# Optimization experiments

Hardware: AMD Instinct MI355X
Metric: run time of the kernel (lower is better)

The kernel has to match this reference:

```python
import jax, jax.numpy as jnp
import numpy as np

GROUPS = 32
EPS = 1e-6


def group_norm(x, gamma, beta):
    # x: [B,H,W,C], NHWC group norm with 32 groups (tfa.layers.GroupNormalization)
    B, H, W, C = x.shape
    g = x.reshape(B, H, W, GROUPS, C // GROUPS)
    mean = g.mean(axis=(1, 2, 4), keepdims=True)
    var = g.var(axis=(1, 2, 4), keepdims=True)
    g = (g - mean) * jax.lax.rsqrt(var + EPS)
    return g.reshape(B, H, W, C) * gamma + beta


def setup_inputs() -> dict:
    key = jax.random.key(0)
    ks = jax.random.split(key, 8)
    B, H, W, C = 8, 64, 64, 64
    s = 1.0 / np.sqrt(C)
    return {
        "x": jax.random.normal(ks[0], (B, H, W, C), jnp.float32),
        "gamma": jnp.ones((C,), jnp.float32),
        "beta": jnp.zeros((C,), jnp.float32),
        "Wq": jax.random.normal(ks[1], (C, C), jnp.float32) * s,
        "bq": jnp.zeros((C,), jnp.float32),
        "Wk": jax.random.normal(ks[2], (C, C), jnp.float32) * s,
        "bk": jnp.zeros((C,), jnp.float32),
        "Wv": jax.random.normal(ks[3], (C, C), jnp.float32) * s,
        "bv": jnp.zeros((C,), jnp.float32),
        "Wp": jax.random.normal(ks[4], (C, C), jnp.float32) * s,
        "bp": jnp.zeros((C,), jnp.float32),
    }


def reference(x, gamma, beta, Wq, bq, Wk, bk, Wv, bv, Wp, bp):
    B, H, W, C = x.shape
    h = group_norm(x, gamma, beta)
    q = h @ Wq + bq            # 1x1 conv (nin) projections, [B,H,W,C]
    k = h @ Wk + bk
    v = h @ Wv + bv
    scale = jnp.asarray(C, x.dtype) ** -0.5
    # full spatial self-attention over flattened HW grid
    w = jnp.einsum('bhwc,bHWc->bhwHW', q, k) * scale
    w = jax.nn.softmax(w.reshape(B, H, W, H * W), axis=-1).reshape(B, H, W, H, W)
    h = jnp.einsum('bhwHW,bHWc->bhwc', w, v)
    h = h @ Wp + bp
    return x + h
```

## Files before the change

### kernel.cpp

```cpp
#include <hip/hip_runtime.h>


typedef __bf16 bf16x8 __attribute__((ext_vector_type(8)));
typedef float f32x16 __attribute__((ext_vector_type(16)));
typedef unsigned u32x2 __attribute__((ext_vector_type(2)));

static __device__ __forceinline__ unsigned short f2b(float f) {
  union { __bf16 b; unsigned short u; } c; c.b = (__bf16)f; return c.u;
}
static __device__ __forceinline__ float b2f(unsigned short u) {
  union { float f; unsigned u; } c; c.u = ((unsigned)u) << 16; return c.f;
}
static __device__ __forceinline__ unsigned pack2(float lo, float hi_) {
  return ((unsigned)f2b(hi_) << 16) | (unsigned)f2b(lo);
}
static __device__ __forceinline__ int a_off(int t, int c) {
  return ((t >> 5) * 4 + (c >> 4)) * 512 + ((t & 31) + 32 * ((c >> 3) & 1)) * 8 + (c & 7);
}
static __device__ __forceinline__ int b_off(int o, int d) {
  return ((o >> 5) * 4 + (d >> 4)) * 512 + ((o & 31) + 32 * ((d >> 3) & 1)) * 8 + (d & 7);
}

__global__ __launch_bounds__(256) void k_part(const float* __restrict__ x,
                                              float* __restrict__ part) {
  const int b = blockIdx.y, ch = blockIdx.x, tid = threadIdx.x;
  const size_t base = ((size_t)(b * 4096 + ch * 128)) * 64;
  float s0 = 0.f, q0 = 0.f, s1 = 0.f, q1 = 0.f;
#pragma unroll
  for (int it = 0; it < 8; ++it) {
    const float4 v = *(const float4*)&x[base + (size_t)tid * 4 + (size_t)it * 1024];
    s0 += v.x + v.y; q0 += v.x * v.x + v.y * v.y;
    s1 += v.z + v.w; q1 += v.z * v.z + v.w * v.w;
  }
  for (int m = 16; m < 64; m <<= 1) {
    s0 += __shfl_xor(s0, m); q0 += __shfl_xor(q0, m);
    s1 += __shfl_xor(s1, m); q1 += __shfl_xor(q1, m);
  }
  __shared__ float red[4][16][4];
  const int lane = tid & 63, wv = tid >> 6;
  if (lane < 16) {
    red[wv][lane][0] = s0; red[wv][lane][1] = q0;
    red[wv][lane][2] = s1; red[wv][lane][3] = q1;
  }
  __syncthreads();
  if (tid < 64) {
    const int ci = tid >> 2, sel = tid & 3;
    const float v = red[0][ci][sel] + red[1][ci][sel] +
                    red[2][ci][sel] + red[3][ci][sel];
    const int g = ci * 2 + (sel >> 1);
    part[(((size_t)b * 32 + g) * 32 + ch) * 2 + (sel & 1)] = v;
  }
}

__global__ __launch_bounds__(256) void k_gnqkv(
    const float* __restrict__ x, const float* __restrict__ gamma,
    const float* __restrict__ beta,
    const float* __restrict__ Wq, const float* __restrict__ bq,
    const float* __restrict__ Wk, const float* __restrict__ bk,
    const float* __restrict__ Wv, const float* __restrict__ bv,
    const float* __restrict__ part,
    unsigned short* __restrict__ qo, unsigned short* __restrict__ ko,
    unsigned short* __restrict__ vo) {
  __shared__ unsigned short hA[4096];
  __shared__ unsigned short WB[3][4096];
  __shared__ float2 stl[32];
  const int b = blockIdx.y, tid = threadIdx.x, t0 = blockIdx.x * 64;

  if (tid < 32) {
    const float* p = part + ((size_t)(b * 32 + tid)) * 64;
    float s = 0.f, q = 0.f;
#pragma unroll
    for (int c4 = 0; c4 < 16; ++c4) {
      const float4 v = *(const float4*)&p[c4 * 4];
      s += v.x + v.z; q += v.y + v.w;
    }
    const float mean = s * (1.0f / 8192.0f);
    const float var = fmaxf(q * (1.0f / 8192.0f) - mean * mean, 0.0f);
    stl[tid] = make_float2(mean, rsqrtf(var + 1e-6f));
  }
  {
    const float* Ws[3] = {Wq, Wk, Wv};
#pragma unroll
    for (int m = 0; m < 3; ++m)
#pragma unroll
      for (int it = 0; it < 4; ++it) {
        const int idx = tid * 4 + it * 1024;
        const int d = idx >> 6, o0 = idx & 63;
        const float4 wv = *(const float4*)&Ws[m][d * 64 + o0];
        WB[m][b_off(o0 + 0, d)] = f2b(wv.x);
        WB[m][b_off(o0 + 1, d)] = f2b(wv.y);
        WB[m][b_off(o0 + 2, d)] = f2b(wv.z);
        WB[m][b_off(o0 + 3, d)] = f2b(wv.w);
      }
  }
  __syncthreads();

#pragma unroll
  for (int it = 0; it < 4; ++it) {
    const int idx = tid * 4 + it * 1024;
    const int tl = idx >> 6, c0 = idx & 63;
    const float4 xv = *(const float4*)&x[((size_t)(b * 4096 + t0 + tl)) * 64 + c0];
    const float2 s0 = stl[(c0 >> 1)];
    const float2 s1 = stl[(c0 >> 1) + 1];
    const float4 gm = *(const float4*)&gamma[c0];
    const float4 bt = *(const float4*)&beta[c0];
    ushort4 hv;
    hv.x = f2b((xv.x - s0.x) * s0.y * gm.x + bt.x);
    hv.y = f2b((xv.y - s0.x) * s0.y * gm.y + bt.y);
    hv.z = f2b((xv.z - s1.x) * s1.y * gm.z + bt.z);
    hv.w = f2b((xv.w - s1.x) * s1.y * gm.w + bt.w);
    *(ushort4*)&hA[a_off(tl, c0)] = hv;
  }
  __syncthreads();

  const int w = tid >> 6, lane = tid & 63;
  const int mt = w >> 1, nt = w & 1, hi = lane >> 5;
  bf16x8 af[4];
#pragma unroll
  for (int cc = 0; cc < 4; ++cc)
    af[cc] = *(const bf16x8*)&hA[(mt * 4 + cc) * 512 + lane * 8];
  f32x16 acc[3];
#pragma unroll
  for (int m = 0; m < 3; ++m)
#pragma unroll
    for (int i = 0; i < 16; ++i) acc[m][i] = 0.f;
#pragma unroll
  for (int m = 0; m < 3; ++m)
#pragma unroll
    for (int cc = 0; cc < 4; ++cc) {
      const bf16x8 bf = *(const bf16x8*)&WB[m][(nt * 4 + cc) * 512 + lane * 8];
      acc[m] = __builtin_amdgcn_mfma_f32_32x32x16_bf16(af[cc], bf, acc[m], 0, 0, 0);
    }

  const int o = 32 * nt + (lane & 31);
  const float bqv = bq[o], bkv = bk[o], bvv = bv[o];
  const float SQ = 0.18033688011112042f;
  const size_t ktile = ((size_t)(b * 64 + blockIdx.x)) * 4096;
#pragma unroll
  for (int r = 0; r < 16; ++r) {
    const int tok = 32 * mt + (r & 3) + 8 * (r >> 2) + 4 * hi;
    const size_t gt = (size_t)(b * 4096 + t0 + tok);
    qo[gt * 64 + o] = f2b((acc[0][r] + bqv) * SQ);
    ko[ktile + ((tok >> 5) * 4 + (o >> 4)) * 512 +
       ((tok & 31) + 32 * ((o >> 3) & 1)) * 8 + (o & 7)] = f2b(acc[1][r] + bkv);
  }
  __syncthreads();
#pragma unroll
  for (int r = 0; r < 16; ++r) {
    const int tok = 32 * mt + (r & 3) + 8 * (r >> 2) + 4 * hi;
    hA[tok * 64 + o] = f2b(acc[2][r] + bvv);
  }
  __syncthreads();
#pragma unroll
  for (int half = 0; half < 2; ++half) {
    const int base = tid * 8 + half * 2048;
    const int sub = base >> 9, lp = (base >> 3) & 63;
    const int db = sub >> 2, ks = sub & 3;
    const int d = 32 * db + (lp & 31);
    const int k6b = 16 * ks + 8 * (lp >> 5);
    uint4 g;
    g.x = ((unsigned)hA[(k6b + 1) * 64 + d] << 16) | hA[(k6b + 0) * 64 + d];
    g.y = ((unsigned)hA[(k6b + 3) * 64 + d] << 16) | hA[(k6b + 2) * 64 + d];
    g.z = ((unsigned)hA[(k6b + 5) * 64 + d] << 16) | hA[(k6b + 4) * 64 + d];
    g.w = ((unsigned)hA[(k6b + 7) * 64 + d] << 16) | hA[(k6b + 6) * 64 + d];
    *(uint4*)&vo[ktile + base] = g;
  }
}

__global__ __launch_bounds__(512, 2) void k_attn(
    const unsigned short* __restrict__ qg, const unsigned short* __restrict__ Kg,
    const unsigned short* __restrict__ Vg,
    float* __restrict__ lb, float* __restrict__ outp) {
  __shared__ unsigned short KV[2][2][8192];
  __shared__ float lred[4][64];
  const int qt = blockIdx.x, sp = blockIdx.y, b = blockIdx.z;
  const int tid = threadIdx.x, w = tid >> 6, lane = tid & 63;
  const int h = w >> 2, p = w & 3;
  const int q32 = lane & 31, hi = lane >> 5;
  const int qrow = qt * 128 + p * 32 + q32;
  const int tid4 = tid & 255;
  const int wq = p;

  bf16x8 qf[4];
  {
    const unsigned short* qsrc = qg + ((size_t)(b * 4096 + qrow)) * 64 + 8 * hi;
#pragma unroll
    for (int cc = 0; cc < 4; ++cc) qf[cc] = *(const bf16x8*)(qsrc + cc * 16);
  }

  f32x16 o[2];
#pragma unroll
  for (int i = 0; i < 16; ++i) { o[0][i] = 0.f; o[1][i] = 0.f; }
  float lrun = 0.f;

  const unsigned short* kgb = Kg + ((size_t)(b * 64 + sp * 32 + h * 16)) * 4096;
  const unsigned short* vgb = Vg + ((size_t)(b * 64 + sp * 32 + h * 16)) * 4096;

  auto STAGE = [&](int tt) {
    const int buf = tt & 1;
    const unsigned short* ks = kgb + (size_t)tt * 4096 + (size_t)tid4 * 8;
    const unsigned short* vs = vgb + (size_t)tt * 4096 + (size_t)tid4 * 8;
    __builtin_amdgcn_global_load_lds(
        (const __attribute__((address_space(1))) void*)ks,
        (__attribute__((address_space(3))) void*)&KV[h][buf][wq * 512], 16, 0, 0);
    __builtin_amdgcn_global_load_lds(
        (const __attribute__((address_space(1))) void*)(ks + 2048),
        (__attribute__((address_space(3))) void*)&KV[h][buf][2048 + wq * 512], 16, 0, 0);
    __builtin_amdgcn_global_load_lds(
        (const __attribute__((address_space(1))) void*)vs,
        (__attribute__((address_space(3))) void*)&KV[h][buf][4096 + wq * 512], 16, 0, 0);
    __builtin_amdgcn_global_load_lds(
        (const __attribute__((address_space(1))) void*)(vs + 2048),
        (__attribute__((address_space(3))) void*)&KV[h][buf][4096 + 2048 + wq * 512], 16, 0, 0);
  };

  STAGE(0);

  for (int t = 0; t < 16; ++t) {
    asm volatile("s_waitcnt vmcnt(0)" ::: "memory");
    __syncthreads();
    __builtin_amdgcn_sched_barrier(0);
    if (t < 15) STAGE(t + 1);

    const int buf = t & 1;
    const unsigned short* Kl = &KV[h][buf][0];
    const unsigned short* Vl = &KV[h][buf][4096];

    f32x16 st0, st1;
#pragma unroll
    for (int i = 0; i < 16; ++i) { st0[i] = 0.f; st1[i] = 0.f; }
    __builtin_amdgcn_s_setprio(1);
#pragma unroll
    for (int cc = 0; cc < 4; ++cc) {
      const bf16x8 a0 = *(const bf16x8*)&Kl[(0 * 4 + cc) * 512 + lane * 8];
      st0 = __builtin_amdgcn_mfma_f32_32x32x16_bf16(a0, qf[cc], st0, 0, 0, 0);
      const bf16x8 a1 = *(const bf16x8*)&Kl[(1 * 4 + cc) * 512 + lane * 8];
      st1 = __builtin_amdgcn_mfma_f32_32x32x16_bf16(a1, qf[cc], st1, 0, 0, 0);
    }
    __builtin_amdgcn_s_setprio(0);

    float rs0 = 0.f, rs1 = 0.f;
#pragma unroll
    for (int r = 0; r < 16; ++r) {
      st0[r] = __builtin_amdgcn_exp2f(st0[r]); rs0 += st0[r];
      st1[r] = __builtin_amdgcn_exp2f(st1[r]); rs1 += st1[r];
    }
    lrun += rs0 + rs1;

    __builtin_amdgcn_s_setprio(1);
#pragma unroll
    for (int t2 = 0; t2 < 2; ++t2) {
      unsigned pk[8];
#pragma unroll
      for (int i = 0; i < 8; ++i)
        pk[i] = t2 ? pack2(st1[2 * i], st1[2 * i + 1])
                   : pack2(st0[2 * i], st0[2 * i + 1]);
#pragma unroll
      for (int s = 0; s < 2; ++s) {
        union { bf16x8 v; unsigned u[4]; } fr;
#if __has_builtin(__builtin_amdgcn_permlane32_swap)
        const u32x2 r02 = __builtin_amdgcn_permlane32_swap(pk[4 * s + 0], pk[4 * s + 2], false, false);
        const u32x2 r13 = __builtin_amdgcn_permlane32_swap(pk[4 * s + 1], pk[4 * s + 3], false, false);
        fr.u[0] = r02[0]; fr.u[1] = r13[0]; fr.u[2] = r02[1]; fr.u[3] = r13[1];
#else
        const unsigned u0 = __shfl_xor(hi ? pk[4 * s + 0] : pk[4 * s + 2], 32);
        const unsigned u1 = __shfl_xor(hi ? pk[4 * s + 1] : pk[4 * s + 3], 32);
        fr.u[0] = hi ? u0 : pk[4 * s + 0];
        fr.u[1] = hi ? u1 : pk[4 * s + 1];
        fr.u[2] = hi ? pk[4 * s + 2] : u0;
        fr.u[3] = hi ? pk[4 * s + 3] : u1;
#endif
        const int kc = t2 * 2 + s;
        const bf16x8 v0 = *(const bf16x8*)&Vl[(0 * 4 + kc) * 512 + lane * 8];
        o[0] = __builtin_amdgcn_mfma_f32_32x32x16_bf16(v0, fr.v, o[0], 0, 0, 0);
        const bf16x8 v1 = *(const bf16x8*)&Vl[(1 * 4 + kc) * 512 + lane * 8];
        o[1] = __builtin_amdgcn_mfma_f32_32x32x16_bf16(v1, fr.v, o[1], 0, 0, 0);
      }
    }
    __builtin_amdgcn_s_setprio(0);
  }

  __syncthreads();
  float* cb = (float*)&KV[0][0][0];
  if (h == 1) {
#pragma unroll
    for (int db = 0; db < 2; ++db)
#pragma unroll
      for (int i = 0; i < 16; ++i)
        cb[p * 2048 + (db * 16 + i) * 64 + lane] = o[db][i];
    lred[p][lane] = lrun;
  }
  __syncthreads();
  if (h == 0) {
#pragma unroll
    for (int db = 0; db < 2; ++db)
#pragma unroll
      for (int i = 0; i < 16; ++i)
        o[db][i] += cb[p * 2048 + (db * 16 + i) * 64 + lane];
    lrun += lred[p][lane];
    lrun += __shfl_xor(lrun, 32);

    char* ob = (char*)outp + ((size_t)(b * 4096 + qrow)) * 256 + sp * 128;
#pragma unroll
    for (int db = 0; db < 2; ++db)
#pragma unroll
      for (int u = 0; u < 4; ++u) {
        ushort4 s;
        s.x = f2b(o[db][4 * u + 0]); s.y = f2b(o[db][4 * u + 1]);
        s.z = f2b(o[db][4 * u + 2]); s.w = f2b(o[db][4 * u + 3]);
        *(ushort4*)(ob + (size_t)(32 * db + 8 * u + 4 * hi) * 2) = s;
      }
    if (hi == 0) lb[((size_t)(b * 2) + sp) * 4096 + qrow] = lrun;
  }
}

__global__ __launch_bounds__(256) void k_comb(
    const float* __restrict__ Wp, const float* __restrict__ bp,
    const float* __restrict__ x, const float* __restrict__ lb,
    float* __restrict__ out) {
  __shared__ unsigned short hA[4096];
  __shared__ unsigned short WB[4096];
  const int b = blockIdx.y, tid = threadIdx.x, t0 = blockIdx.x * 64;

#pragma unroll
  for (int it = 0; it < 4; ++it) {
    const int idx = tid * 4 + it * 1024;
    const int d = idx >> 6, o0 = idx & 63;
    const float4 wv = *(const float4*)&Wp[d * 64 + o0];
    WB[b_off(o0 + 0, d)] = f2b(wv.x);
    WB[b_off(o0 + 1, d)] = f2b(wv.y);
    WB[b_off(o0 + 2, d)] = f2b(wv.z);
    WB[b_off(o0 + 3, d)] = f2b(wv.w);
  }
#pragma unroll
  for (int it = 0; it < 4; ++it) {
    const int idx = tid * 4 + it * 1024;
    const int tl = idx >> 6, d0 = idx & 63;
    const int trow = t0 + tl;
    const size_t gt = (size_t)(b * 4096 + trow);
    const float lsum = lb[((size_t)b * 2 + 0) * 4096 + trow] +
                       lb[((size_t)b * 2 + 1) * 4096 + trow];
    const float invL = 1.0f / lsum;
    const char* pb = (const char*)out + gt * 256;
    const ushort4 p0 = *(const ushort4*)(pb + (size_t)d0 * 2);
    const ushort4 p1 = *(const ushort4*)(pb + 128 + (size_t)d0 * 2);
    ushort4 hv;
    hv.x = f2b((b2f(p0.x) + b2f(p1.x)) * invL);
    hv.y = f2b((b2f(p0.y) + b2f(p1.y)) * invL);
    hv.z = f2b((b2f(p0.z) + b2f(p1.z)) * invL);
    hv.w = f2b((b2f(p0.w) + b2f(p1.w)) * invL);
    *(ushort4*)&hA[a_off(tl, d0)] = hv;
  }
  __syncthreads();

  const int w = tid >> 6, lane = tid & 63;
  const int mt = w >> 1, nt = w & 1, hi = lane >> 5;
  f32x16 acc2;
#pragma unroll
  for (int i = 0; i < 16; ++i) acc2[i] = 0.f;
#pragma unroll
  for (int cc = 0; cc < 4; ++cc) {
    const bf16x8 a = *(const bf16x8*)&hA[(mt * 4 + cc) * 512 + lane * 8];
    const bf16x8 bf = *(const bf16x8*)&WB[(nt * 4 + cc) * 512 + lane * 8];
    acc2 = __builtin_amdgcn_mfma_f32_32x32x16_bf16(a, bf, acc2, 0, 0, 0);
  }
  const int o = 32 * nt + (lane & 31);
  const float bpv = bp[o];
#pragma unroll
  for (int r = 0; r < 16; ++r) {
    const int tok = 32 * mt + (r & 3) + 8 * (r >> 2) + 4 * hi;
    const size_t gt = (size_t)(b * 4096 + t0 + tok);
    out[gt * 64 + o] = acc2[r] + bpv + x[gt * 64 + o];
  }
}

extern "C" void kernel_launch(void* const* d_in, const int* in_sizes, int n_in,
                              void* d_out, int out_size, void* d_ws,
                              size_t ws_size, hipStream_t stream) {
  const float* x     = (const float*)d_in[0];
  const float* gamma = (const float*)d_in[1];
  const float* beta  = (const float*)d_in[2];
  const float* Wq    = (const float*)d_in[3];
  const float* bq    = (const float*)d_in[4];
  const float* Wk    = (const float*)d_in[5];
  const float* bk    = (const float*)d_in[6];
  const float* Wv    = (const float*)d_in[7];
  const float* bv    = (const float*)d_in[8];
  const float* Wp    = (const float*)d_in[9];
  const float* bp    = (const float*)d_in[10];
  float* out = (float*)d_out;

  char* ws = (char*)d_ws;
  float* part = (float*)ws;
  float* lbuf = (float*)ws;
  unsigned short* qb = (unsigned short*)(ws + 524288);
  unsigned short* kb = qb + (size_t)8 * 4096 * 64;
  unsigned short* vb = kb + (size_t)8 * 4096 * 64;

  k_part<<<dim3(32, 8), 256, 0, stream>>>(x, part);
  k_gnqkv<<<dim3(64, 8), 256, 0, stream>>>(x, gamma, beta, Wq, bq, Wk, bk, Wv,
                                           bv, part, qb, kb, vb);
  k_attn<<<dim3(32, 2, 8), 512, 0, stream>>>(qb, kb, vb, lbuf, out);
  k_comb<<<dim3(64, 8), 256, 0, stream>>>(Wp, bp, x, lbuf, out);
}
```

Before: 68.29 us.

## Process two 32-row query subtiles per warp to reuse K/V fragments

Each warp in the attention kernel now handles 64 query rows (two 32-row subtiles) instead of 32. Every K and V fragment read from LDS feeds two MFMAs, which halves LDS traffic and global K/V staging per query. The grid shrinks to 16 query tiles per batch and split. This roughly doubles accumulator register use and halves the block count, so occupancy and the 2-blocks-per-CU launch bound may suffer. The epilogue reduction buffer is resized to match.

```diff
diff --git a/kernel.cpp b/kernel.cpp
--- a/kernel.cpp
+++ b/kernel.cpp
@@ -10,9 +10,6 @@
 }
 static __device__ __forceinline__ float b2f(unsigned short u) {
   union { float f; unsigned u; } c; c.u = ((unsigned)u) << 16; return c.f;
-}
-static __device__ __forceinline__ unsigned pack2(float lo, float hi_) {
-  return ((unsigned)f2b(hi_) << 16) | (unsigned)f2b(lo);
 }
 static __device__ __forceinline__ int a_off(int t, int c) {
   return ((t >> 5) * 4 + (c >> 4)) * 512 + ((t & 31) + 32 * ((c >> 3) & 1)) * 8 + (c & 7);
@@ -172,26 +169,29 @@
     const unsigned short* __restrict__ Vg,
     float* __restrict__ lb, float* __restrict__ outp) {
   __shared__ unsigned short KV[2][2][8192];
-  __shared__ float lred[4][64];
+  __shared__ float lred[4][2][64];
   const int qt = blockIdx.x, sp = blockIdx.y, b = blockIdx.z;
   const int tid = threadIdx.x, w = tid >> 6, lane = tid & 63;
   const int h = w >> 2, p = w & 3;
   const int q32 = lane & 31, hi = lane >> 5;
-  const int qrow = qt * 128 + p * 32 + q32;
   const int tid4 = tid & 255;
   const int wq = p;
 
-  bf16x8 qf[4];
-  {
-    const unsigned short* qsrc = qg + ((size_t)(b * 4096 + qrow)) * 64 + 8 * hi;
-#pragma unroll
-    for (int cc = 0; cc < 4; ++cc) qf[cc] = *(const bf16x8*)(qsrc + cc * 16);
-  }
-
-  f32x16 o[2];
-#pragma unroll
-  for (int i = 0; i < 16; ++i) { o[0][i] = 0.f; o[1][i] = 0.f; }
-  float lrun = 0.f;
+  bf16x8 qf[2][4];
+#pragma unroll
+  for (int qs = 0; qs < 2; ++qs) {
+    const unsigned short* qsrc =
+        qg + ((size_t)(b * 4096 + qt * 256 + p * 64 + qs * 32 + q32)) * 64 + 8 * hi;
+#pragma unroll
+    for (int cc = 0; cc < 4; ++cc) qf[qs][cc] = *(const bf16x8*)(qsrc + cc * 16);
+  }
+
+  f32x16 o[2][2];
+#pragma unroll
+  for (int qs = 0; qs < 2; ++qs)
+#pragma unroll
+    for (int i = 0; i < 16; ++i) { o[qs][0][i] = 0.f; o[qs][1][i] = 0.f; }
+  float lrun[2] = {0.f, 0.f};
 
   const unsigned short* kgb = Kg + ((size_t)(b * 64 + sp * 32 + h * 16)) * 4096;
   const unsigned short* vgb = Vg + ((size_t)(b * 64 + sp * 32 + h * 16)) * 4096;
@@ -226,57 +226,73 @@
     const unsigned short* Kl = &KV[h][buf][0];
     const unsigned short* Vl = &KV[h][buf][4096];
 
-    f32x16 st0, st1;
-#pragma unroll
-    for (int i = 0; i < 16; ++i) { st0[i] = 0.f; st1[i] = 0.f; }
+    f32x16 st[2][2];
+#pragma unroll
+    for (int qs = 0; qs < 2; ++qs)
+#pragma unroll
+      for (int i = 0; i < 16; ++i) { st[qs][0][i] = 0.f; st[qs][1][i] = 0.f; }
     __builtin_amdgcn_s_setprio(1);
 #pragma unroll
     for (int cc = 0; cc < 4; ++cc) {
-      const bf16x8 a0 = *(const bf16x8*)&Kl[(0 * 4 + cc) * 512 + lane * 8];
-      st0 = __builtin_amdgcn_mfma_f32_32x32x16_bf16(a0, qf[cc], st0, 0, 0, 0);
-      const bf16x8 a1 = *(const bf16x8*)&Kl[(1 * 4 + cc) * 512 + lane * 8];
-      st1 = __builtin_amdgcn_mfma_f32_32x32x16_bf16(a1, qf[cc], st1, 0, 0, 0);
+      const bf16x8 a0 = *(const bf16x8*)&Kl[cc * 512 + lane * 8];
+      const bf16x8 a1 = *(const bf16x8*)&Kl[(4 + cc) * 512 + lane * 8];
+      st[0][0] = __builtin_amdgcn_mfma_f32_32x32x16_bf16(a0, qf[0][cc], st[0][0], 0, 0, 0);
+      st[1][0] = __builtin_amdgcn_mfma_f32_32x32x16_bf16(a0, qf[1][cc], st[1][0], 0, 0, 0);
+      st[0][1] = __builtin_amdgcn_mfma_f32_32x32x16_bf16(a1, qf[0][cc], st[0][1], 0, 0, 0);
+      st[1][1] = __builtin_amdgcn_mfma_f32_32x32x16_bf16(a1, qf[1][cc], st[1][1], 0, 0, 0);
     }
     __builtin_amdgcn_s_setprio(0);
 
-    float rs0 = 0.f, rs1 = 0.f;
-#pragma unroll
-    for (int r = 0; r < 16; ++r) {
-      st0[r] = __builtin_amdgcn_exp2f(st0[r]); rs0 += st0[r];
-      st1[r] = __builtin_amdgcn_exp2f(st1[r]); rs1 += st1[r];
-    }
-    lrun += rs0 + rs1;
+    union PK { unsigned u[8]; __bf16 e[16]; } pk[2][2];
+#pragma unroll
+    for (int qs = 0; qs < 2; ++qs) {
+      float r0 = 0.f, r1 = 0.f, r2 = 0.f, r3 = 0.f;
+#pragma unroll
+      for (int ks = 0; ks < 2; ++ks)
+#pragma unroll
+        for (int i = 0; i < 16; i += 4) {
+          const float e0 = __builtin_amdgcn_exp2f(st[qs][ks][i + 0]);
+          const float e1 = __builtin_amdgcn_exp2f(st[qs][ks][i + 1]);
+          const float e2 = __builtin_amdgcn_exp2f(st[qs][ks][i + 2]);
+          const float e3 = __builtin_amdgcn_exp2f(st[qs][ks][i + 3]);
+          r0 += e0; r1 += e1; r2 += e2; r3 += e3;
+          pk[qs][ks].e[i + 0] = (__bf16)e0; pk[qs][ks].e[i + 1] = (__bf16)e1;
+          pk[qs][ks].e[i + 2] = (__bf16)e2; pk[qs][ks].e[i + 3] = (__bf16)e3;
+        }
+      lrun[qs] += (r0 + r1) + (r2 + r3);
+    }
 
     __builtin_amdgcn_s_setprio(1);
 #pragma unroll
-    for (int t2 = 0; t2 < 2; ++t2) {
-      unsigned pk[8];
-#pragma unroll
-      for (int i = 0; i < 8; ++i)
-        pk[i] = t2 ? pack2(st1[2 * i], st1[2 * i + 1])
-                   : pack2(st0[2 * i], st0[2 * i + 1]);
+    for (int ks = 0; ks < 2; ++ks)
 #pragma unroll
       for (int s = 0; s < 2; ++s) {
-        union { bf16x8 v; unsigned u[4]; } fr;
+        const int kc = ks * 2 + s;
+        const bf16x8 v0 = *(const bf16x8*)&Vl[kc * 512 + lane * 8];
+        const bf16x8 v1 = *(const bf16x8*)&Vl[(4 + kc) * 512 + lane * 8];
+#pragma unroll
+        for (int qs = 0; qs < 2; ++qs) {
+          union { bf16x8 v; unsigned u[4]; } fr;
 #if __has_builtin(__builtin_amdgcn_permlane32_swap)
-        const u32x2 r02 = __builtin_amdgcn_permlane32_swap(pk[4 * s + 0], pk[4 * s + 2], false, false);
-        const u32x2 r13 = __builtin_amdgcn_permlane32_swap(pk[4 * s + 1], pk[4 * s + 3], false, false);
-        fr.u[0] = r02[0]; fr.u[1] = r13[0]; fr.u[2] = r02[1]; fr.u[3] = r13[1];
+          const u32x2 r02 = __builtin_amdgcn_permlane32_swap(
+              pk[qs][ks].u[4 * s + 0], pk[qs][ks].u[4 * s + 2], false, false);
+          const u32x2 r13 = __builtin_amdgcn_permlane32_swap(
+              pk[qs][ks].u[4 * s + 1], pk[qs][ks].u[4 * s + 3], false, false);
+          fr.u[0] = r02[0]; fr.u[1] = r13[0]; fr.u[2] = r02[1]; fr.u[3] = r13[1];
 #else
-        const unsigned u0 = __shfl_xor(hi ? pk[4 * s + 0] : pk[4 * s + 2], 32);
-        const unsigned u1 = __shfl_xor(hi ? pk[4 * s + 1] : pk[4 * s + 3], 32);
-        fr.u[0] = hi ? u0 : pk[4 * s + 0];
-        fr.u[1] = hi ? u1 : pk[4 * s + 1];
-        fr.u[2] = hi ? pk[4 * s + 2] : u0;
-        fr.u[3] = hi ? pk[4 * s + 3] : u1;
+          const unsigned u0 =
+              __shfl_xor(hi ? pk[qs][ks].u[4 * s + 0] : pk[qs][ks].u[4 * s + 2], 32);
+          const unsigned u1 =
+              __shfl_xor(hi ? pk[qs][ks].u[4 * s + 1] : pk[qs][ks].u[4 * s + 3], 32);
+          fr.u[0] = hi ? u0 : pk[qs][ks].u[4 * s + 0];
+          fr.u[1] = hi ? u1 : pk[qs][ks].u[4 * s + 1];
+          fr.u[2] = hi ? pk[qs][ks].u[4 * s + 2] : u0;
+          fr.u[3] = hi ? pk[qs][ks].u[4 * s + 3] : u1;
 #endif
-        const int kc = t2 * 2 + s;
-        const bf16x8 v0 = *(const bf16x8*)&Vl[(0 * 4 + kc) * 512 + lane * 8];
-        o[0] = __builtin_amdgcn_mfma_f32_32x32x16_bf16(v0, fr.v, o[0], 0, 0, 0);
-        const bf16x8 v1 = *(const bf16x8*)&Vl[(1 * 4 + kc) * 512 + lane * 8];
-        o[1] = __builtin_amdgcn_mfma_f32_32x32x16_bf16(v1, fr.v, o[1], 0, 0, 0);
+          o[qs][0] = __builtin_amdgcn_mfma_f32_32x32x16_bf16(v0, fr.v, o[qs][0], 0, 0, 0);
+          o[qs][1] = __builtin_amdgcn_mfma_f32_32x32x16_bf16(v1, fr.v, o[qs][1], 0, 0, 0);
+        }
       }
-    }
     __builtin_amdgcn_s_setprio(0);
   }
 
@@ -284,33 +300,40 @@
   float* cb = (float*)&KV[0][0][0];
   if (h == 1) {
 #pragma unroll
-    for (int db = 0; db < 2; ++db)
-#pragma unroll
-      for (int i = 0; i < 16; ++i)
-        cb[p * 2048 + (db * 16 + i) * 64 + lane] = o[db][i];
-    lred[p][lane] = lrun;
+    for (int qs = 0; qs < 2; ++qs) {
+#pragma unroll
+      for (int db = 0; db < 2; ++db)
+#pragma unroll
+        for (int i = 0; i < 16; ++i)
+          cb[(p * 2 + qs) * 2048 + (db * 16 + i) * 64 + lane] = o[qs][db][i];
+      lred[p][qs][lane] = lrun[qs];
+    }
   }
   __syncthreads();
   if (h == 0) {
 #pragma unroll
-    for (int db = 0; db < 2; ++db)
-#pragma unroll
-      for (int i = 0; i < 16; ++i)
-        o[db][i] += cb[p * 2048 + (db * 16 + i) * 64 + lane];
-    lrun += lred[p][lane];
-    lrun += __shfl_xor(lrun, 32);
-
-    char* ob = (char*)outp + ((size_t)(b * 4096 + qrow)) * 256 + sp * 128;
-#pragma unroll
-    for (int db = 0; db < 2; ++db)
-#pragma unroll
-      for (int u = 0; u < 4; ++u) {
-        ushort4 s;
-        s.x = f2b(o[db][4 * u + 0]); s.y = f2b(o[db][4 * u + 1]);
-        s.z = f2b(o[db][4 * u + 2]); s.w = f2b(o[db][4 * u + 3]);
-        *(ushort4*)(ob + (size_t)(32 * db + 8 * u + 4 * hi) * 2) = s;
-      }
-    if (hi == 0) lb[((size_t)(b * 2) + sp) * 4096 + qrow] = lrun;
+    for (int qs = 0; qs < 2; ++qs) {
+#pragma unroll
+      for (int db = 0; db < 2; ++db)
+#pragma unroll
+        for (int i = 0; i < 16; ++i)
+          o[qs][db][i] += cb[(p * 2 + qs) * 2048 + (db * 16 + i) * 64 + lane];
+      float lq = lrun[qs] + lred[p][qs][lane];
+      lq += __shfl_xor(lq, 32);
+
+      const int qrow = qt * 256 + p * 64 + qs * 32 + q32;
+      char* ob = (char*)outp + ((size_t)(b * 4096 + qrow)) * 256 + sp * 128;
+#pragma unroll
+      for (int db = 0; db < 2; ++db)
+#pragma unroll
+        for (int u = 0; u < 4; ++u) {
+          ushort4 s;
+          s.x = f2b(o[qs][db][4 * u + 0]); s.y = f2b(o[qs][db][4 * u + 1]);
+          s.z = f2b(o[qs][db][4 * u + 2]); s.w = f2b(o[qs][db][4 * u + 3]);
+          *(ushort4*)(ob + (size_t)(32 * db + 8 * u + 4 * hi) * 2) = s;
+        }
+      if (hi == 0) lb[((size_t)(b * 2) + sp) * 4096 + qrow] = lq;
+    }
   }
 }
 
@@ -400,6 +423,6 @@
   k_part<<<dim3(32, 8), 256, 0, stream>>>(x, part);
   k_gnqkv<<<dim3(64, 8), 256, 0, stream>>>(x, gamma, beta, Wq, bq, Wk, bk, Wv,
                                            bv, part, qb, kb, vb);
-  k_attn<<<dim3(32, 2, 8), 512, 0, stream>>>(qb, kb, vb, lbuf, out);
+  k_attn<<<dim3(16, 2, 8), 512, 0, stream>>>(qb, kb, vb, lbuf, out);
   k_comb<<<dim3(64, 8), 256, 0, stream>>>(Wp, bp, x, lbuf, out);
 }
```

Measured after the change: 68.92 us. No clear change (+0.9%).

## Software-pipeline QK and PV across tiles in attention kernel, MFMA row sums

Applied to the files above, without the earlier changes.

Restructures the attention loop so the QK^T MFMAs for the next tile are issued before the softmax and PV MFMAs of the current tile, using two sets of score registers in a two-step unrolled loop. V fragments are preloaded into registers before each PV step. The softmax denominator is now accumulated by an extra MFMA against a ones matrix, which replaces the scalar exp-sum and the lane shuffle, and it sums the bf16-rounded probabilities. The grid is remapped so that batch and split vary fastest. In exchange there are more barriers per tile, higher register pressure, and one extra MFMA per PV step.

```diff
diff --git a/kernel.cpp b/kernel.cpp
--- a/kernel.cpp
+++ b/kernel.cpp
@@ -20,6 +20,10 @@
 static __device__ __forceinline__ int b_off(int o, int d) {
   return ((o >> 5) * 4 + (d >> 4)) * 512 + ((o & 31) + 32 * ((d >> 3) & 1)) * 8 + (d & 7);
 }
+
+#define GLL(src, dst) __builtin_amdgcn_global_load_lds(                        \
+    (const __attribute__((address_space(1))) void*)(src),                     \
+    (__attribute__((address_space(3))) void*)(dst), 16, 0, 0)
 
 __global__ __launch_bounds__(256) void k_part(const float* __restrict__ x,
                                               float* __restrict__ part) {
@@ -173,13 +177,13 @@
     float* __restrict__ lb, float* __restrict__ outp) {
   __shared__ unsigned short KV[2][2][8192];
   __shared__ float lred[4][64];
-  const int qt = blockIdx.x, sp = blockIdx.y, b = blockIdx.z;
+  const int bs = blockIdx.x, qt = blockIdx.y;
+  const int b = bs >> 1, sp = bs & 1;
   const int tid = threadIdx.x, w = tid >> 6, lane = tid & 63;
   const int h = w >> 2, p = w & 3;
   const int q32 = lane & 31, hi = lane >> 5;
   const int qrow = qt * 128 + p * 32 + q32;
-  const int tid4 = tid & 255;
-  const int wq = p;
+  const int tid4 = tid & 255, wq = p;
 
   bf16x8 qf[4];
   {
@@ -187,11 +191,14 @@
 #pragma unroll
     for (int cc = 0; cc < 4; ++cc) qf[cc] = *(const bf16x8*)(qsrc + cc * 16);
   }
-
-  f32x16 o[2];
-#pragma unroll
-  for (int i = 0; i < 16; ++i) { o[0][i] = 0.f; o[1][i] = 0.f; }
-  float lrun = 0.f;
+  bf16x8 onesA;
+  { union { unsigned u[4]; bf16x8 v; } c;
+    c.u[0] = c.u[1] = c.u[2] = c.u[3] = 0x3f803f80u; onesA = c.v; }
+
+  f32x16 o0, o1, lacc;
+#pragma unroll
+  for (int i = 0; i < 16; ++i) { o0[i] = 0.f; o1[i] = 0.f; lacc[i] = 0.f; }
+  f32x16 stA0, stA1, stB0, stB1;
 
   const unsigned short* kgb = Kg + ((size_t)(b * 64 + sp * 32 + h * 16)) * 4096;
   const unsigned short* vgb = Vg + ((size_t)(b * 64 + sp * 32 + h * 16)) * 4096;
@@ -200,117 +207,130 @@
     const int buf = tt & 1;
     const unsigned short* ks = kgb + (size_t)tt * 4096 + (size_t)tid4 * 8;
     const unsigned short* vs = vgb + (size_t)tt * 4096 + (size_t)tid4 * 8;
-    __builtin_amdgcn_global_load_lds(
-        (const __attribute__((address_space(1))) void*)ks,
-        (__attribute__((address_space(3))) void*)&KV[h][buf][wq * 512], 16, 0, 0);
-    __builtin_amdgcn_global_load_lds(
-        (const __attribute__((address_space(1))) void*)(ks + 2048),
-        (__attribute__((address_space(3))) void*)&KV[h][buf][2048 + wq * 512], 16, 0, 0);
-    __builtin_amdgcn_global_load_lds(
-        (const __attribute__((address_space(1))) void*)vs,
-        (__attribute__((address_space(3))) void*)&KV[h][buf][4096 + wq * 512], 16, 0, 0);
-    __builtin_amdgcn_global_load_lds(
-        (const __attribute__((address_space(1))) void*)(vs + 2048),
-        (__attribute__((address_space(3))) void*)&KV[h][buf][4096 + 2048 + wq * 512], 16, 0, 0);
+    GLL(ks, &KV[h][buf][wq * 512]);
+    GLL(ks + 2048, &KV[h][buf][2048 + wq * 512]);
+    GLL(vs, &KV[h][buf][4096 + wq * 512]);
+    GLL(vs + 2048, &KV[h][buf][4096 + 2048 + wq * 512]);
   };
-
-  STAGE(0);
-
-  for (int t = 0; t < 16; ++t) {
-    asm volatile("s_waitcnt vmcnt(0)" ::: "memory");
-    __syncthreads();
-    __builtin_amdgcn_sched_barrier(0);
-    if (t < 15) STAGE(t + 1);
-
-    const int buf = t & 1;
+  auto QK = [&](int buf, f32x16& s0, f32x16& s1) {
     const unsigned short* Kl = &KV[h][buf][0];
+#pragma unroll
+    for (int i = 0; i < 16; ++i) { s0[i] = 0.f; s1[i] = 0.f; }
+    __builtin_amdgcn_s_setprio(1);
+#pragma unroll
+    for (int cc = 0; cc < 4; ++cc) {
+      const bf16x8 a0 = *(const bf16x8*)&Kl[cc * 512 + lane * 8];
+      const bf16x8 a1 = *(const bf16x8*)&Kl[(4 + cc) * 512 + lane * 8];
+      s0 = __builtin_amdgcn_mfma_f32_32x32x16_bf16(a0, qf[cc], s0, 0, 0, 0);
+      s1 = __builtin_amdgcn_mfma_f32_32x32x16_bf16(a1, qf[cc], s1, 0, 0, 0);
+    }
+    __builtin_amdgcn_s_setprio(0);
+  };
+  auto LOADV = [&](int buf, bf16x8* vf) {
     const unsigned short* Vl = &KV[h][buf][4096];
-
-    f32x16 st0, st1;
-#pragma unroll
-    for (int i = 0; i < 16; ++i) { st0[i] = 0.f; st1[i] = 0.f; }
+#pragma unroll
+    for (int j = 0; j < 8; ++j) vf[j] = *(const bf16x8*)&Vl[j * 512 + lane * 8];
+  };
+  auto SMPV = [&](f32x16& sc0, f32x16& sc1, const bf16x8* vf) {
+    unsigned pk[2][8];
+#pragma unroll
+    for (int ks = 0; ks < 2; ++ks) {
+      const f32x16& s = ks ? sc1 : sc0;
+#pragma unroll
+      for (int i = 0; i < 8; ++i) {
+        const float e0 = __builtin_amdgcn_exp2f(s[2 * i]);
+        const float e1 = __builtin_amdgcn_exp2f(s[2 * i + 1]);
+        pk[ks][i] = pack2(e0, e1);
+      }
+    }
     __builtin_amdgcn_s_setprio(1);
 #pragma unroll
-    for (int cc = 0; cc < 4; ++cc) {
-      const bf16x8 a0 = *(const bf16x8*)&Kl[(0 * 4 + cc) * 512 + lane * 8];
-      st0 = __builtin_amdgcn_mfma_f32_32x32x16_bf16(a0, qf[cc], st0, 0, 0, 0);
-      const bf16x8 a1 = *(const bf16x8*)&Kl[(1 * 4 + cc) * 512 + lane * 8];
-      st1 = __builtin_amdgcn_mfma_f32_32x32x16_bf16(a1, qf[cc], st1, 0, 0, 0);
-    }
-    __builtin_amdgcn_s_setprio(0);
-
-    float rs0 = 0.f, rs1 = 0.f;
-#pragma unroll
-    for (int r = 0; r < 16; ++r) {
-      st0[r] = __builtin_amdgcn_exp2f(st0[r]); rs0 += st0[r];
-      st1[r] = __builtin_amdgcn_exp2f(st1[r]); rs1 += st1[r];
-    }
-    lrun += rs0 + rs1;
-
-    __builtin_amdgcn_s_setprio(1);
-#pragma unroll
-    for (int t2 = 0; t2 < 2; ++t2) {
-      unsigned pk[8];
-#pragma unroll
-      for (int i = 0; i < 8; ++i)
-        pk[i] = t2 ? pack2(st1[2 * i], st1[2 * i + 1])
-                   : pack2(st0[2 * i], st0[2 * i + 1]);
+    for (int ks = 0; ks < 2; ++ks)
 #pragma unroll
       for (int s = 0; s < 2; ++s) {
         union { bf16x8 v; unsigned u[4]; } fr;
 #if __has_builtin(__builtin_amdgcn_permlane32_swap)
-        const u32x2 r02 = __builtin_amdgcn_permlane32_swap(pk[4 * s + 0], pk[4 * s + 2], false, false);
-        const u32x2 r13 = __builtin_amdgcn_permlane32_swap(pk[4 * s + 1], pk[4 * s + 3], false, false);
+        const u32x2 r02 = __builtin_amdgcn_permlane32_swap(
+            pk[ks][4 * s + 0], pk[ks][4 * s + 2], false, false);
+        const u32x2 r13 = __builtin_amdgcn_permlane32_swap(
+            pk[ks][4 * s + 1], pk[ks][4 * s + 3], false, false);
         fr.u[0] = r02[0]; fr.u[1] = r13[0]; fr.u[2] = r02[1]; fr.u[3] = r13[1];
 #else
-        const unsigned u0 = __shfl_xor(hi ? pk[4 * s + 0] : pk[4 * s + 2], 32);
-        const unsigned u1 = __shfl_xor(hi ? pk[4 * s + 1] : pk[4 * s + 3], 32);
-        fr.u[0] = hi ? u0 : pk[4 * s + 0];
-        fr.u[1] = hi ? u1 : pk[4 * s + 1];
-        fr.u[2] = hi ? pk[4 * s + 2] : u0;
-        fr.u[3] = hi ? pk[4 * s + 3] : u1;
+        const unsigned u0 = __shfl_xor(hi ? pk[ks][4 * s + 0] : pk[ks][4 * s + 2], 32);
+        const unsigned u1 = __shfl_xor(hi ? pk[ks][4 * s + 1] : pk[ks][4 * s + 3], 32);
+        fr.u[0] = hi ? u0 : pk[ks][4 * s + 0];
+        fr.u[1] = hi ? u1 : pk[ks][4 * s + 1];
+        fr.u[2] = hi ? pk[ks][4 * s + 2] : u0;
+        fr.u[3] = hi ? pk[ks][4 * s + 3] : u1;
 #endif
-        const int kc = t2 * 2 + s;
-        const bf16x8 v0 = *(const bf16x8*)&Vl[(0 * 4 + kc) * 512 + lane * 8];
-        o[0] = __builtin_amdgcn_mfma_f32_32x32x16_bf16(v0, fr.v, o[0], 0, 0, 0);
-        const bf16x8 v1 = *(const bf16x8*)&Vl[(1 * 4 + kc) * 512 + lane * 8];
-        o[1] = __builtin_amdgcn_mfma_f32_32x32x16_bf16(v1, fr.v, o[1], 0, 0, 0);
+        const int kc = ks * 2 + s;
+        lacc = __builtin_amdgcn_mfma_f32_32x32x16_bf16(onesA, fr.v, lacc, 0, 0, 0);
+        o0 = __builtin_amdgcn_mfma_f32_32x32x16_bf16(vf[kc], fr.v, o0, 0, 0, 0);
+        o1 = __builtin_amdgcn_mfma_f32_32x32x16_bf16(vf[4 + kc], fr.v, o1, 0, 0, 0);
       }
-    }
     __builtin_amdgcn_s_setprio(0);
+  };
+
+  STAGE(0);
+  asm volatile("s_waitcnt vmcnt(0)" ::: "memory");
+  __syncthreads();
+  STAGE(1);
+  QK(0, stA0, stA1);
+
+  bf16x8 vf[8];
+#pragma unroll 1
+  for (int t = 0; t < 16; t += 2) {
+    asm volatile("s_waitcnt vmcnt(0)" ::: "memory");
+    __syncthreads();
+    if (t + 1 < 16) QK((t + 1) & 1, stB0, stB1);
+    LOADV(t & 1, vf);
+    asm volatile("s_waitcnt lgkmcnt(0)" ::: "memory");
+    __syncthreads();
+    if (t + 2 < 16) STAGE(t + 2);
+    SMPV(stA0, stA1, vf);
+
+    asm volatile("s_waitcnt vmcnt(0)" ::: "memory");
+    __syncthreads();
+    if (t + 2 < 16) QK((t + 2) & 1, stA0, stA1);
+    LOADV((t + 1) & 1, vf);
+    asm volatile("s_waitcnt lgkmcnt(0)" ::: "memory");
+    __syncthreads();
+    if (t + 3 < 16) STAGE(t + 3);
+    SMPV(stB0, stB1, vf);
   }
 
   __syncthreads();
   float* cb = (float*)&KV[0][0][0];
   if (h == 1) {
 #pragma unroll
-    for (int db = 0; db < 2; ++db)
-#pragma unroll
-      for (int i = 0; i < 16; ++i)
-        cb[p * 2048 + (db * 16 + i) * 64 + lane] = o[db][i];
-    lred[p][lane] = lrun;
+    for (int i = 0; i < 16; ++i) {
+      cb[p * 2048 + i * 64 + lane] = o0[i];
+      cb[p * 2048 + (16 + i) * 64 + lane] = o1[i];
+    }
+    lred[p][lane] = lacc[0];
   }
   __syncthreads();
   if (h == 0) {
 #pragma unroll
-    for (int db = 0; db < 2; ++db)
-#pragma unroll
-      for (int i = 0; i < 16; ++i)
-        o[db][i] += cb[p * 2048 + (db * 16 + i) * 64 + lane];
-    lrun += lred[p][lane];
-    lrun += __shfl_xor(lrun, 32);
+    for (int i = 0; i < 16; ++i) {
+      o0[i] += cb[p * 2048 + i * 64 + lane];
+      o1[i] += cb[p * 2048 + (16 + i) * 64 + lane];
+    }
+    const float lq = lacc[0] + lred[p][lane];
 
     char* ob = (char*)outp + ((size_t)(b * 4096 + qrow)) * 256 + sp * 128;
 #pragma unroll
-    for (int db = 0; db < 2; ++db)
+    for (int db = 0; db < 2; ++db) {
+      const f32x16& ov = db ? o1 : o0;
 #pragma unroll
       for (int u = 0; u < 4; ++u) {
         ushort4 s;
-        s.x = f2b(o[db][4 * u + 0]); s.y = f2b(o[db][4 * u + 1]);
-        s.z = f2b(o[db][4 * u + 2]); s.w = f2b(o[db][4 * u + 3]);
+        s.x = f2b(ov[4 * u + 0]); s.y = f2b(ov[4 * u + 1]);
+        s.z = f2b(ov[4 * u + 2]); s.w = f2b(ov[4 * u + 3]);
         *(ushort4*)(ob + (size_t)(32 * db + 8 * u + 4 * hi) * 2) = s;
       }
-    if (hi == 0) lb[((size_t)(b * 2) + sp) * 4096 + qrow] = lrun;
+    }
+    if (hi == 0) lb[((size_t)(b * 2) + sp) * 4096 + qrow] = lq;
   }
 }
 
@@ -400,6 +420,6 @@
   k_part<<<dim3(32, 8), 256, 0, stream>>>(x, part);
   k_gnqkv<<<dim3(64, 8), 256, 0, stream>>>(x, gamma, beta, Wq, bq, Wk, bk, Wv,
                                            bv, part, qb, kb, vb);
-  k_attn<<<dim3(32, 2, 8), 512, 0, stream>>>(qb, kb, vb, lbuf, out);
+  k_attn<<<dim3(16, 32), 512, 0, stream>>>(qb, kb, vb, lbuf, out);
   k_comb<<<dim3(64, 8), 256, 0, stream>>>(Wp, bp, x, lbuf, out);
 }
```

After: 73.85 us. +8.2%, slower.

## Restructure attention kernel into single-group 4-wave blocks with software-pipelined K/V staging

Applied to the files above, without the earlier changes.

The attention kernel drops the two-half split of each block (two groups of 4 waves, each covering half the keys and merged at the end through LDS). It now uses 256-thread blocks in which each wave walks all 32 key tiles of its split. K is double-buffered and V triple-buffered, and the next tile's QK MFMA is issued before the barrier wait so it overlaps the softmax/PV of the current tile. This removes the final cross-half reduction and its extra syncs, and grid ordering changes so batch/split vary fastest. The cost is a longer serial loop per wave and more LDS per block relative to threads.

```diff
diff --git a/kernel.cpp b/kernel.cpp
--- a/kernel.cpp
+++ b/kernel.cpp
@@ -11,15 +11,16 @@
 static __device__ __forceinline__ float b2f(unsigned short u) {
   union { float f; unsigned u; } c; c.u = ((unsigned)u) << 16; return c.f;
 }
-static __device__ __forceinline__ unsigned pack2(float lo, float hi_) {
-  return ((unsigned)f2b(hi_) << 16) | (unsigned)f2b(lo);
-}
 static __device__ __forceinline__ int a_off(int t, int c) {
   return ((t >> 5) * 4 + (c >> 4)) * 512 + ((t & 31) + 32 * ((c >> 3) & 1)) * 8 + (c & 7);
 }
 static __device__ __forceinline__ int b_off(int o, int d) {
   return ((o >> 5) * 4 + (d >> 4)) * 512 + ((o & 31) + 32 * ((d >> 3) & 1)) * 8 + (d & 7);
 }
+
+#define GLL(src, dst) __builtin_amdgcn_global_load_lds(                        \
+    (const __attribute__((address_space(1))) void*)(src),                     \
+    (__attribute__((address_space(3))) void*)(dst), 16, 0, 0)
 
 __global__ __launch_bounds__(256) void k_part(const float* __restrict__ x,
                                               float* __restrict__ part) {
@@ -167,19 +168,17 @@
   }
 }
 
-__global__ __launch_bounds__(512, 2) void k_attn(
+__global__ __launch_bounds__(256, 4) void k_attn(
     const unsigned short* __restrict__ qg, const unsigned short* __restrict__ Kg,
     const unsigned short* __restrict__ Vg,
     float* __restrict__ lb, float* __restrict__ outp) {
-  __shared__ unsigned short KV[2][2][8192];
-  __shared__ float lred[4][64];
-  const int qt = blockIdx.x, sp = blockIdx.y, b = blockIdx.z;
+  __shared__ unsigned short Klds[2][4096];
+  __shared__ unsigned short Vlds[3][4096];
+  const int bs = blockIdx.x, qt = blockIdx.y;
+  const int b = bs >> 1, sp = bs & 1;
   const int tid = threadIdx.x, w = tid >> 6, lane = tid & 63;
-  const int h = w >> 2, p = w & 3;
   const int q32 = lane & 31, hi = lane >> 5;
-  const int qrow = qt * 128 + p * 32 + q32;
-  const int tid4 = tid & 255;
-  const int wq = p;
+  const int qrow = qt * 128 + w * 32 + q32;
 
   bf16x8 qf[4];
   {
@@ -188,130 +187,115 @@
     for (int cc = 0; cc < 4; ++cc) qf[cc] = *(const bf16x8*)(qsrc + cc * 16);
   }
 
-  f32x16 o[2];
-#pragma unroll
-  for (int i = 0; i < 16; ++i) { o[0][i] = 0.f; o[1][i] = 0.f; }
+  f32x16 o0, o1, st0, st1;
+#pragma unroll
+  for (int i = 0; i < 16; ++i) { o0[i] = 0.f; o1[i] = 0.f; }
   float lrun = 0.f;
 
-  const unsigned short* kgb = Kg + ((size_t)(b * 64 + sp * 32 + h * 16)) * 4096;
-  const unsigned short* vgb = Vg + ((size_t)(b * 64 + sp * 32 + h * 16)) * 4096;
-
-  auto STAGE = [&](int tt) {
-    const int buf = tt & 1;
-    const unsigned short* ks = kgb + (size_t)tt * 4096 + (size_t)tid4 * 8;
-    const unsigned short* vs = vgb + (size_t)tt * 4096 + (size_t)tid4 * 8;
-    __builtin_amdgcn_global_load_lds(
-        (const __attribute__((address_space(1))) void*)ks,
-        (__attribute__((address_space(3))) void*)&KV[h][buf][wq * 512], 16, 0, 0);
-    __builtin_amdgcn_global_load_lds(
-        (const __attribute__((address_space(1))) void*)(ks + 2048),
-        (__attribute__((address_space(3))) void*)&KV[h][buf][2048 + wq * 512], 16, 0, 0);
-    __builtin_amdgcn_global_load_lds(
-        (const __attribute__((address_space(1))) void*)vs,
-        (__attribute__((address_space(3))) void*)&KV[h][buf][4096 + wq * 512], 16, 0, 0);
-    __builtin_amdgcn_global_load_lds(
-        (const __attribute__((address_space(1))) void*)(vs + 2048),
-        (__attribute__((address_space(3))) void*)&KV[h][buf][4096 + 2048 + wq * 512], 16, 0, 0);
+  const unsigned short* kgb = Kg + ((size_t)(b * 64 + sp * 32)) * 4096;
+  const unsigned short* vgb = Vg + ((size_t)(b * 64 + sp * 32)) * 4096;
+
+  auto STAGE_K = [&](int tt, int buf) {
+    const unsigned short* ks = kgb + (size_t)tt * 4096 + (size_t)tid * 8;
+    GLL(ks, &Klds[buf][w * 512]);
+    GLL(ks + 2048, &Klds[buf][2048 + w * 512]);
   };
-
-  STAGE(0);
-
-  for (int t = 0; t < 16; ++t) {
-    asm volatile("s_waitcnt vmcnt(0)" ::: "memory");
-    __syncthreads();
-    __builtin_amdgcn_sched_barrier(0);
-    if (t < 15) STAGE(t + 1);
-
-    const int buf = t & 1;
-    const unsigned short* Kl = &KV[h][buf][0];
-    const unsigned short* Vl = &KV[h][buf][4096];
-
-    f32x16 st0, st1;
+  auto STAGE_V = [&](int tt, int buf) {
+    const unsigned short* vs = vgb + (size_t)tt * 4096 + (size_t)tid * 8;
+    GLL(vs, &Vlds[buf][w * 512]);
+    GLL(vs + 2048, &Vlds[buf][2048 + w * 512]);
+  };
+  auto QK = [&](int buf) {
 #pragma unroll
     for (int i = 0; i < 16; ++i) { st0[i] = 0.f; st1[i] = 0.f; }
     __builtin_amdgcn_s_setprio(1);
 #pragma unroll
     for (int cc = 0; cc < 4; ++cc) {
-      const bf16x8 a0 = *(const bf16x8*)&Kl[(0 * 4 + cc) * 512 + lane * 8];
+      const bf16x8 a0 = *(const bf16x8*)&Klds[buf][cc * 512 + lane * 8];
+      const bf16x8 a1 = *(const bf16x8*)&Klds[buf][(4 + cc) * 512 + lane * 8];
       st0 = __builtin_amdgcn_mfma_f32_32x32x16_bf16(a0, qf[cc], st0, 0, 0, 0);
-      const bf16x8 a1 = *(const bf16x8*)&Kl[(1 * 4 + cc) * 512 + lane * 8];
       st1 = __builtin_amdgcn_mfma_f32_32x32x16_bf16(a1, qf[cc], st1, 0, 0, 0);
     }
     __builtin_amdgcn_s_setprio(0);
-
-    float rs0 = 0.f, rs1 = 0.f;
-#pragma unroll
-    for (int r = 0; r < 16; ++r) {
-      st0[r] = __builtin_amdgcn_exp2f(st0[r]); rs0 += st0[r];
-      st1[r] = __builtin_amdgcn_exp2f(st1[r]); rs1 += st1[r];
-    }
-    lrun += rs0 + rs1;
-
-    __builtin_amdgcn_s_setprio(1);
-#pragma unroll
-    for (int t2 = 0; t2 < 2; ++t2) {
-      unsigned pk[8];
-#pragma unroll
-      for (int i = 0; i < 8; ++i)
-        pk[i] = t2 ? pack2(st1[2 * i], st1[2 * i + 1])
-                   : pack2(st0[2 * i], st0[2 * i + 1]);
-#pragma unroll
-      for (int s = 0; s < 2; ++s) {
+  };
+
+  STAGE_K(0, 0); STAGE_V(0, 0);
+  STAGE_K(1, 1); STAGE_V(1, 1);
+  STAGE_V(2, 2);
+  asm volatile("s_waitcnt vmcnt(2)" ::: "memory");
+  __builtin_amdgcn_s_barrier();
+  QK(0);
+
+  int kb_ = 0, vb_ = 0;
+#pragma unroll 1
+  for (int t = 0; t < 32; ++t) {
+#pragma unroll
+    for (int ks2 = 0; ks2 < 2; ++ks2) {
+      const f32x16 s = ks2 ? st1 : st0;
+      union { unsigned u[8]; __bf16 e[16]; } pku;
+      float l0 = 0.f, l1 = 0.f, l2 = 0.f, l3 = 0.f;
+#pragma unroll
+      for (int i = 0; i < 16; i += 4) {
+        const float e0 = __builtin_amdgcn_exp2f(s[i + 0]);
+        const float e1 = __builtin_amdgcn_exp2f(s[i + 1]);
+        const float e2 = __builtin_amdgcn_exp2f(s[i + 2]);
+        const float e3 = __builtin_amdgcn_exp2f(s[i + 3]);
+        l0 += e0; l1 += e1; l2 += e2; l3 += e3;
+        pku.e[i + 0] = (__bf16)e0; pku.e[i + 1] = (__bf16)e1;
+        pku.e[i + 2] = (__bf16)e2; pku.e[i + 3] = (__bf16)e3;
+      }
+      lrun += (l0 + l1) + (l2 + l3);
+      __builtin_amdgcn_s_setprio(1);
+#pragma unroll
+      for (int sbl = 0; sbl < 2; ++sbl) {
         union { bf16x8 v; unsigned u[4]; } fr;
 #if __has_builtin(__builtin_amdgcn_permlane32_swap)
-        const u32x2 r02 = __builtin_amdgcn_permlane32_swap(pk[4 * s + 0], pk[4 * s + 2], false, false);
-        const u32x2 r13 = __builtin_amdgcn_permlane32_swap(pk[4 * s + 1], pk[4 * s + 3], false, false);
+        const u32x2 r02 = __builtin_amdgcn_permlane32_swap(
+            pku.u[4 * sbl + 0], pku.u[4 * sbl + 2], false, false);
+        const u32x2 r13 = __builtin_amdgcn_permlane32_swap(
+            pku.u[4 * sbl + 1], pku.u[4 * sbl + 3], false, false);
         fr.u[0] = r02[0]; fr.u[1] = r13[0]; fr.u[2] = r02[1]; fr.u[3] = r13[1];
 #else
-        const unsigned u0 = __shfl_xor(hi ? pk[4 * s + 0] : pk[4 * s + 2], 32);
-        const unsigned u1 = __shfl_xor(hi ? pk[4 * s + 1] : pk[4 * s + 3], 32);
-        fr.u[0] = hi ? u0 : pk[4 * s + 0];
-        fr.u[1] = hi ? u1 : pk[4 * s + 1];
-        fr.u[2] = hi ? pk[4 * s + 2] : u0;
-        fr.u[3] = hi ? pk[4 * s + 3] : u1;
+        const unsigned u0 = __shfl_xor(hi ? pku.u[4 * sbl + 0] : pku.u[4 * sbl + 2], 32);
+        const unsigned u1 = __shfl_xor(hi ? pku.u[4 * sbl + 1] : pku.u[4 * sbl + 3], 32);
+        fr.u[0] = hi ? u0 : pku.u[4 * sbl + 0];
+        fr.u[1] = hi ? u1 : pku.u[4 * sbl + 1];
+        fr.u[2] = hi ? pku.u[4 * sbl + 2] : u0;
+        fr.u[3] = hi ? pku.u[4 * sbl + 3] : u1;
 #endif
-        const int kc = t2 * 2 + s;
-        const bf16x8 v0 = *(const bf16x8*)&Vl[(0 * 4 + kc) * 512 + lane * 8];
-        o[0] = __builtin_amdgcn_mfma_f32_32x32x16_bf16(v0, fr.v, o[0], 0, 0, 0);
-        const bf16x8 v1 = *(const bf16x8*)&Vl[(1 * 4 + kc) * 512 + lane * 8];
-        o[1] = __builtin_amdgcn_mfma_f32_32x32x16_bf16(v1, fr.v, o[1], 0, 0, 0);
+        const int kc = ks2 * 2 + sbl;
+        const bf16x8 v0 = *(const bf16x8*)&Vlds[vb_][kc * 512 + lane * 8];
+        const bf16x8 v1 = *(const bf16x8*)&Vlds[vb_][(4 + kc) * 512 + lane * 8];
+        o0 = __builtin_amdgcn_mfma_f32_32x32x16_bf16(v0, fr.v, o0, 0, 0, 0);
+        o1 = __builtin_amdgcn_mfma_f32_32x32x16_bf16(v1, fr.v, o1, 0, 0, 0);
       }
-    }
-    __builtin_amdgcn_s_setprio(0);
-  }
-
-  __syncthreads();
-  float* cb = (float*)&KV[0][0][0];
-  if (h == 1) {
-#pragma unroll
-    for (int db = 0; db < 2; ++db)
-#pragma unroll
-      for (int i = 0; i < 16; ++i)
-        cb[p * 2048 + (db * 16 + i) * 64 + lane] = o[db][i];
-    lred[p][lane] = lrun;
-  }
-  __syncthreads();
-  if (h == 0) {
-#pragma unroll
-    for (int db = 0; db < 2; ++db)
-#pragma unroll
-      for (int i = 0; i < 16; ++i)
-        o[db][i] += cb[p * 2048 + (db * 16 + i) * 64 + lane];
-    lrun += lred[p][lane];
-    lrun += __shfl_xor(lrun, 32);
-
-    char* ob = (char*)outp + ((size_t)(b * 4096 + qrow)) * 256 + sp * 128;
-#pragma unroll
-    for (int db = 0; db < 2; ++db)
-#pragma unroll
-      for (int u = 0; u < 4; ++u) {
-        ushort4 s;
-        s.x = f2b(o[db][4 * u + 0]); s.y = f2b(o[db][4 * u + 1]);
-        s.z = f2b(o[db][4 * u + 2]); s.w = f2b(o[db][4 * u + 3]);
-        *(ushort4*)(ob + (size_t)(32 * db + 8 * u + 4 * hi) * 2) = s;
-      }
-    if (hi == 0) lb[((size_t)(b * 2) + sp) * 4096 + qrow] = lrun;
-  }
+      __builtin_amdgcn_s_setprio(0);
+    }
+
+    asm volatile("s_waitcnt lgkmcnt(0) vmcnt(2)" ::: "memory");
+    __builtin_amdgcn_s_barrier();
+
+    if (t + 2 < 32) STAGE_K(t + 2, kb_);
+    if (t + 3 < 32) STAGE_V(t + 3, vb_);
+    kb_ ^= 1;
+    vb_ = (vb_ == 2) ? 0 : vb_ + 1;
+    if (t + 1 < 32) QK(kb_);
+  }
+
+  lrun += __shfl_xor(lrun, 32);
+  char* ob = (char*)outp + ((size_t)(b * 4096 + qrow)) * 256 + sp * 128;
+#pragma unroll
+  for (int db = 0; db < 2; ++db) {
+    const f32x16& ov = db ? o1 : o0;
+#pragma unroll
+    for (int u = 0; u < 4; ++u) {
+      ushort4 s;
+      s.x = f2b(ov[4 * u + 0]); s.y = f2b(ov[4 * u + 1]);
+      s.z = f2b(ov[4 * u + 2]); s.w = f2b(ov[4 * u + 3]);
+      *(ushort4*)(ob + (size_t)(32 * db + 8 * u + 4 * hi) * 2) = s;
+    }
+  }
+  if (hi == 0) lb[((size_t)(b * 2) + sp) * 4096 + qrow] = lrun;
 }
 
 __global__ __launch_bounds__(256) void k_comb(
@@ -400,6 +384,6 @@
   k_part<<<dim3(32, 8), 256, 0, stream>>>(x, part);
   k_gnqkv<<<dim3(64, 8), 256, 0, stream>>>(x, gamma, beta, Wq, bq, Wk, bk, Wv,
                                            bv, part, qb, kb, vb);
-  k_attn<<<dim3(32, 2, 8), 512, 0, stream>>>(qb, kb, vb, lbuf, out);
+  k_attn<<<dim3(16, 32), 256, 0, stream>>>(qb, kb, vb, lbuf, out);
   k_comb<<<dim3(64, 8), 256, 0, stream>>>(Wp, bp, x, lbuf, out);
 }
```

Result: slower. 84.81 us (+24.2%).
